# Optimization experiments

Hardware: AMD Instinct MI355X
Metric: run time of the kernel (lower is better)

The kernel has to match this reference:

```python
import jax, jax.numpy as jnp
import numpy as np

B, C, L, E = 32, 3, 512, 512


def setup_inputs() -> dict:
    key = jax.random.key(0)
    ks = jax.random.split(key, 13)
    bnd = float(np.sqrt(6.0 / (2.0 * E)))  # xavier-uniform-like bound
    uni = lambda k, shp: jax.random.uniform(k, shp, jnp.float32, -bnd, bnd)
    return {
        "A0": jax.random.normal(ks[0], (B, C, L, L), jnp.float32),
        "x0": jax.random.normal(ks[1], (B, C, L, E), jnp.float32),
        "u0": jax.random.normal(ks[2], (B, C, E), jnp.float32),
        "t0": jax.random.normal(ks[3], (B, E), jnp.float32),
        "t1": jax.random.normal(ks[4], (B, E), jnp.float32),
        "Q_weight": uni(ks[5], (C, E, E)),
        "Q_bias": jnp.zeros((C, E), jnp.float32),
        "V_weight": uni(ks[6], (C, E, E)),
        "V_bias": jnp.zeros((C, E), jnp.float32),
        "K_weight": uni(ks[7], (C, E, E)),
        "K_bias": jnp.zeros((C, E), jnp.float32),
        "T_weight": uni(ks[8], (C, E, E)),
        "T_bias": jnp.zeros((C, E), jnp.float32),
    }


def reference(A0, x0, u0, t0, t1,
              Q_weight, Q_bias, V_weight, V_bias,
              K_weight, K_bias, T_weight, T_bias):
    # Time embeddings: (B,E) @ (C,E,E) -> (B,C,E)
    T0 = jnp.einsum('be,cef->bcf', t0, T_weight)
    T1 = jnp.einsum('be,cef->bcf', t1, T_weight)

    # Original modulates weight columns: x @ (W * T) == (x @ W) * T (T broadcasts
    # over the input axis via unsqueeze(-2)); use the fused, equivalent form.
    Q = jnp.einsum('bce,cef->bcf', x0[:, :, -1, :], Q_weight) * T0 + Q_bias  # (B,C,E)
    K = jnp.einsum('bce,cef->bcf', u0, K_weight) * T1 + K_bias               # (B,C,E)
    V = jnp.einsum('bcle,cef->bclf', x0, V_weight) * T1[:, :, None, :] \
        + V_bias[None, :, None, :]                                           # (B,C,L,E)

    QKV = jax.nn.softmax(jnp.einsum('bce,bcle->bcl', Q * K, V), axis=-1)     # (B,C,L)

    # A1[:, :, i, :] = A0[:, :, i+1, :] - A0[:, :, 0, :] for i < L-1;
    # A1[:, :, L-1, :] = A1[:, :, L-2, :] + QKV  (= A0[-1] - A0[0] + QKV)
    rows = A0[:, :, 1:, :] - A0[:, :, :1, :]                                 # (B,C,L-1,L)
    last = rows[:, :, -1, :] + QKV                                           # (B,C,L)
    A1 = jnp.concatenate([rows, last[:, :, None, :]], axis=2)                # (B,C,L,L)

    x1 = jnp.einsum('bclm,bcme->bcle', A1, x0)                               # (B,C,L,E)
    x1 = jnp.diff(x1, axis=2, prepend=jnp.zeros_like(x1[:, :, :1, :]))

    num = jnp.sum(T0 * T1, axis=-1)                                          # (B,C)
    den = jnp.sqrt(jnp.sum(T0 * T0, axis=-1) + jnp.sum(T1 * T1, axis=-1))
    w = (num / den)[..., None]                                               # (B,C,1)

    u1 = u0 * (1.0 - w) + x1.mean(axis=-2) * w                               # (B,C,E)
    return (A1 - A0, x1 - x0, u1 - u0)
```

## Files before the change

kernel.cpp:

```cpp
#include <hip/hip_runtime.h>
#include <stdint.h>

#define BB 32
#define CC 3
#define LL 512
#define EE 512
#define NBC (BB*CC)

#define O2_OFF ((size_t)NBC*LL*LL)
#define O3_OFF (O2_OFF + (size_t)NBC*LL*EE)

#define WSB_QX    0
#define WSB_H     196608
#define WSB_W     442368
#define WSB_ADIFF ((size_t)512*1024)
#define ADIFF_BYTES ((size_t)NBC*LL*LL*2)
#define WSB_X0T   (WSB_ADIFF + ADIFF_BYTES)
#define WS_FAST_NEED (WSB_X0T + ADIFF_BYTES)

#define NEC 16

typedef short bf16x8 __attribute__((ext_vector_type(8)));
typedef float f32x4  __attribute__((ext_vector_type(4)));

__device__ __forceinline__ float wred_sum(float v){
#pragma unroll
  for (int m = 32; m >= 1; m >>= 1) v += __shfl_xor(v, m, 64);
  return v;
}
__device__ __forceinline__ float wred_max(float v){
#pragma unroll
  for (int m = 32; m >= 1; m >>= 1) v = fmaxf(v, __shfl_xor(v, m, 64));
  return v;
}
__device__ __forceinline__ void f4ma(float4& a, float s, const float4& b){
  a.x = fmaf(s, b.x, a.x); a.y = fmaf(s, b.y, a.y);
  a.z = fmaf(s, b.z, a.z); a.w = fmaf(s, b.w, a.w);
}
__device__ __forceinline__ float4 f4sub(const float4& a, const float4& b){
  return make_float4(a.x-b.x, a.y-b.y, a.z-b.z, a.w-b.w);
}
__device__ __forceinline__ unsigned short f2bf(float x){
  unsigned u = __float_as_uint(x);
  return (unsigned short)((u + 0x7FFFu + ((u >> 16) & 1u)) >> 16);
}
__device__ __forceinline__ float bf2f(unsigned short h){
  return __uint_as_float(((unsigned)h) << 16);
}
__device__ __forceinline__ void split1(float v, unsigned short& hi, unsigned short& lo){
  hi = f2bf(v);
  lo = f2bf(v - bf2f(hi));
}

__global__ __launch_bounds__(512) void k0p(
    const float* __restrict__ x0, const float* __restrict__ u0,
    const float* __restrict__ t0, const float* __restrict__ t1,
    const float* __restrict__ Qw, const float* __restrict__ Kw,
    const float* __restrict__ Tw,
    float* __restrict__ P)
{
  const int bg = blockIdx.x;
  const int c  = blockIdx.y;
  const int ec = blockIdx.z;
  const int b0 = bg*4;
  const int e0 = ec*32;
  const int f  = threadIdx.x;
  __shared__ float vb[4][4][32];
  {
    int vec = f >> 7, j = (f >> 5) & 3, e = f & 31;
    int bb = b0 + j;
    float v;
    if      (vec == 0) v = t0[bb*EE + e0 + e];
    else if (vec == 1) v = t1[bb*EE + e0 + e];
    else if (vec == 2) v = x0[((size_t)(bb*CC + c)*LL + (LL-1))*EE + e0 + e];
    else               v = u0[(size_t)(bb*CC + c)*EE + e0 + e];
    vb[vec][j][e] = v;
  }
  __syncthreads();

  const float* twp = Tw + (size_t)c*EE*EE + (size_t)e0*EE + f;
  const float* qwp = Qw + (size_t)c*EE*EE + (size_t)e0*EE + f;
  const float* kwp = Kw + (size_t)c*EE*EE + (size_t)e0*EE + f;
  float aT0[4]={0,0,0,0}, aT1[4]={0,0,0,0}, aQ[4]={0,0,0,0}, aK[4]={0,0,0,0};
#pragma unroll 8
  for (int e = 0; e < 32; ++e) {
    float wt = twp[(size_t)e*EE];
    float wq = qwp[(size_t)e*EE];
    float wk = kwp[(size_t)e*EE];
#pragma unroll
    for (int j = 0; j < 4; ++j) {
      aT0[j] = fmaf(vb[0][j][e], wt, aT0[j]);
      aT1[j] = fmaf(vb[1][j][e], wt, aT1[j]);
      aQ[j]  = fmaf(vb[2][j][e], wq, aQ[j]);
      aK[j]  = fmaf(vb[3][j][e], wk, aK[j]);
    }
  }
#pragma unroll
  for (int j = 0; j < 4; ++j) {
    int cb = c*BB + b0 + j;
    P[(((size_t)0*NEC + ec)*96 + cb)*EE + f] = aT0[j];
    P[(((size_t)1*NEC + ec)*96 + cb)*EE + f] = aT1[j];
    P[(((size_t)2*NEC + ec)*96 + cb)*EE + f] = aQ[j];
    P[(((size_t)3*NEC + ec)*96 + cb)*EE + f] = aK[j];
  }
}

__global__ __launch_bounds__(512) void k0c(
    const float* __restrict__ P,
    const float* __restrict__ Qb, const float* __restrict__ Kb,
    float* __restrict__ gtbuf, float* __restrict__ ws_w)
{
  const int bc = blockIdx.x;
  const int b = bc / CC, c = bc % CC;
  const int cb = c*BB + b;
  const int f = threadIdx.x;
  const int wid = f >> 6, lane = f & 63;
  __shared__ float red[8][3];
  float aT0=0.f, aT1=0.f, aQ=0.f, aK=0.f;
#pragma unroll
  for (int ec = 0; ec < NEC; ++ec) {
    aT0 += P[(((size_t)0*NEC + ec)*96 + cb)*EE + f];
    aT1 += P[(((size_t)1*NEC + ec)*96 + cb)*EE + f];
    aQ  += P[(((size_t)2*NEC + ec)*96 + cb)*EE + f];
    aK  += P[(((size_t)3*NEC + ec)*96 + cb)*EE + f];
  }
  float Qv = aQ*aT0 + Qb[c*EE + f];
  float Kv = aK*aT1 + Kb[c*EE + f];
  gtbuf[(size_t)cb*EE + f] = Qv*Kv*aT1;
  float pn = wred_sum(aT0*aT1);
  float p0 = wred_sum(aT0*aT0);
  float p1 = wred_sum(aT1*aT1);
  if (lane == 0) { red[wid][0]=pn; red[wid][1]=p0; red[wid][2]=p1; }
  __syncthreads();
  if (f == 0) {
    float sn=0.f, s0=0.f, s1=0.f;
    for (int i=0;i<8;++i){ sn+=red[i][0]; s0+=red[i][1]; s1+=red[i][2]; }
    ws_w[bc] = sn / sqrtf(s0 + s1);
  }
}

__global__ __launch_bounds__(256) void k1_h(
    const float* __restrict__ Vw, const float* __restrict__ gtbuf,
    float* __restrict__ ws_h)
{
  const int nt = blockIdx.x;
  const int c  = blockIdx.y;
  const int n0 = nt*128;
  const int t = threadIdx.x, lane = t & 63, w = t >> 6;
  __shared__ __align__(16) char AgtH[32*1024];
  __shared__ __align__(16) char AgtL[32*1024];
  __shared__ __align__(16) char BvH[128*128];
  __shared__ __align__(16) char BvL[128*128];
  {
    int row = t >> 3, sl = t & 7;
    const float* src = gtbuf + ((size_t)(c*BB + row))*EE + sl*64;
#pragma unroll
    for (int c3 = 0; c3 < 8; ++c3) {
      float4 a = *reinterpret_cast<const float4*>(src + c3*8);
      float4 b = *reinterpret_cast<const float4*>(src + c3*8 + 4);
      ushort4 h0,h1,l0,l1;
      split1(a.x,h0.x,l0.x); split1(a.y,h0.y,l0.y); split1(a.z,h0.z,l0.z); split1(a.w,h0.w,l0.w);
      split1(b.x,h1.x,l1.x); split1(b.y,h1.y,l1.y); split1(b.z,h1.z,l1.z); split1(b.w,h1.w,l1.w);
      int off = row*1024 + sl*128 + ((c3 ^ (row & 7)) << 4);
      *reinterpret_cast<ushort4*>(AgtH + off)     = h0;
      *reinterpret_cast<ushort4*>(AgtH + off + 8) = h1;
      *reinterpret_cast<ushort4*>(AgtL + off)     = l0;
      *reinterpret_cast<ushort4*>(AgtL + off + 8) = l1;
    }
  }
  f32x4 acc[2][2];
#pragma unroll
  for (int mi=0; mi<2; ++mi)
#pragma unroll
    for (int ni=0; ni<2; ++ni) acc[mi][ni] = (f32x4){0.f,0.f,0.f,0.f};

  for (int kk = 0; kk < 8; ++kk) {
    __syncthreads();
    {
      int nl = t >> 1, half = t & 1;
      const float* src = Vw + (size_t)c*EE*EE + (size_t)(n0+nl)*EE + kk*64 + half*32;
#pragma unroll
      for (int q = 0; q < 4; ++q) {
        float4 a = *reinterpret_cast<const float4*>(src + q*8);
        float4 b = *reinterpret_cast<const float4*>(src + q*8 + 4);
        int c3 = half*4 + q;
        ushort4 h0,h1,l0,l1;
        split1(a.x,h0.x,l0.x); split1(a.y,h0.y,l0.y); split1(a.z,h0.z,l0.z); split1(a.w,h0.w,l0.w);
        split1(b.x,h1.x,l1.x); split1(b.y,h1.y,l1.y); split1(b.z,h1.z,l1.z); split1(b.w,h1.w,l1.w);
        int off = nl*128 + ((c3 ^ (nl & 7)) << 4);
        *reinterpret_cast<ushort4*>(BvH + off)     = h0;
        *reinterpret_cast<ushort4*>(BvH + off + 8) = h1;
        *reinterpret_cast<ushort4*>(BvL + off)     = l0;
        *reinterpret_cast<ushort4*>(BvL + off + 8) = l1;
      }
    }
    __syncthreads();
    bf16x8 afH[2][2], afL[2][2], bfH[2][2], bfL[2][2];
#pragma unroll
    for (int mi=0; mi<2; ++mi)
#pragma unroll
      for (int ks=0; ks<2; ++ks) {
        int row = mi*16 + (lane & 15);
        int c3 = ks*4 + (lane >> 4);
        int off = row*1024 + kk*128 + ((c3 ^ (row & 7)) << 4);
        afH[mi][ks] = *reinterpret_cast<const bf16x8*>(AgtH + off);
        afL[mi][ks] = *reinterpret_cast<const bf16x8*>(AgtL + off);
      }
#pragma unroll
    for (int ni=0; ni<2; ++ni)
#pragma unroll
      for (int ks=0; ks<2; ++ks) {
        int n = w*32 + ni*16 + (lane & 15);
        int c3 = ks*4 + (lane >> 4);
        int off = n*128 + ((c3 ^ (n & 7)) << 4);
        bfH[ni][ks] = *reinterpret_cast<const bf16x8*>(BvH + off);
        bfL[ni][ks] = *reinterpret_cast<const bf16x8*>(BvL + off);
      }
#pragma unroll
    for (int mi=0; mi<2; ++mi)
#pragma unroll
      for (int ni=0; ni<2; ++ni)
#pragma unroll
        for (int ks=0; ks<2; ++ks) {
          acc[mi][ni] = __builtin_amdgcn_mfma_f32_16x16x32_bf16(afH[mi][ks], bfH[ni][ks], acc[mi][ni], 0, 0, 0);
          acc[mi][ni] = __builtin_amdgcn_mfma_f32_16x16x32_bf16(afH[mi][ks], bfL[ni][ks], acc[mi][ni], 0, 0, 0);
          acc[mi][ni] = __builtin_amdgcn_mfma_f32_16x16x32_bf16(afL[mi][ks], bfH[ni][ks], acc[mi][ni], 0, 0, 0);
        }
  }
#pragma unroll
  for (int mi=0; mi<2; ++mi)
#pragma unroll
    for (int ni=0; ni<2; ++ni)
#pragma unroll
      for (int r=0; r<4; ++r) {
        int b = mi*16 + (lane >> 4)*4 + r;
        int e = n0 + w*32 + ni*16 + (lane & 15);
        ws_h[((size_t)(b*CC + c))*EE + e] = acc[mi][ni][r];
      }
}

__global__ __launch_bounds__(512) void k2f(
    const float* __restrict__ A0, const float* __restrict__ x0,
    const float* __restrict__ u0,
    const float* __restrict__ ws_h, const float* __restrict__ ws_w,
    float* __restrict__ ws_qx, float* __restrict__ out1, float* __restrict__ out3)
{
  const int bc = blockIdx.x;
  const int tid = threadIdx.x, wid = tid >> 6, lane = tid & 63;
  __shared__ __align__(16) float hb[EE], sb[LL], a0r0[LL], a0r3[LL];
  __shared__ float red[8];
  __shared__ float partl[4][12][128];
  const size_t abase = (size_t)bc*LL*LL;
  const size_t xbase = (size_t)bc*LL*EE;
  hb[tid]   = ws_h[(size_t)bc*EE + tid];
  a0r0[tid] = A0[abase + tid];
  a0r3[tid] = A0[abase + (size_t)(LL-1)*LL + tid];
  __syncthreads();
  const float4 h0 = *reinterpret_cast<const float4*>(&hb[lane*8]);
  const float4 h1 = *reinterpret_cast<const float4*>(&hb[lane*8+4]);
  for (int l = wid; l < LL; l += 8) {
    const float4* xr = reinterpret_cast<const float4*>(x0 + xbase + (size_t)l*EE);
    float4 v0 = xr[lane*2], v1 = xr[lane*2+1];
    float acc = v0.x*h0.x + v0.y*h0.y + v0.z*h0.z + v0.w*h0.w
              + v1.x*h1.x + v1.y*h1.y + v1.z*h1.z + v1.w*h1.w;
    acc = wred_sum(acc);
    if (lane == 0) sb[l] = acc;
  }
  __syncthreads();
  float v = sb[tid];
  float mx = wred_max(v);
  if (lane == 0) red[wid] = mx;
  __syncthreads();
  mx = red[0];
#pragma unroll
  for (int i = 1; i < 8; ++i) mx = fmaxf(mx, red[i]);
  float ev = __expf(v - mx);
  float sm = wred_sum(ev);
  __syncthreads();
  if (lane == 0) red[wid] = sm;
  __syncthreads();
  float tot = 0.f;
#pragma unroll
  for (int i = 0; i < 8; ++i) tot += red[i];
  float qk = ev / tot;
  sb[tid] = qk;
  out1[abase + (size_t)(LL-1)*LL + tid] = qk - a0r0[tid];
  __syncthreads();
  const int mg = tid >> 7, cg = tid & 127;
  float4 aq = make_float4(0,0,0,0), a0s = make_float4(0,0,0,0), a3s = make_float4(0,0,0,0);
#pragma unroll 4
  for (int i = 0; i < 128; ++i) {
    int m = mg*128 + i;
    float4 xv = *reinterpret_cast<const float4*>(x0 + xbase + (size_t)m*EE + cg*4);
    float qm = sb[m], z0 = a0r0[m], z3 = a0r3[m];
    f4ma(aq, qm, xv); f4ma(a0s, z0, xv); f4ma(a3s, z3, xv);
  }
#pragma unroll
  for (int k = 0; k < 4; ++k) {
    partl[mg][0+k][cg] = (&aq.x)[k];
    partl[mg][4+k][cg] = (&a0s.x)[k];
    partl[mg][8+k][cg] = (&a3s.x)[k];
  }
  __syncthreads();
  if (mg == 0) {
    float wv = ws_w[bc];
    float4 uv = *reinterpret_cast<const float4*>(u0 + (size_t)bc*EE + cg*4);
    float4 qx4, o3;
#pragma unroll
    for (int k = 0; k < 4; ++k) {
      float q = 0.f, y0 = 0.f, y3 = 0.f;
#pragma unroll
      for (int g = 0; g < 4; ++g) {
        q  += partl[g][0+k][cg];
        y0 += partl[g][4+k][cg];
        y3 += partl[g][8+k][cg];
      }
      (&qx4.x)[k] = q;
      (&o3.x)[k] = wv * ((y3 - y0 + q) * (1.f/(float)LL) - (&uv.x)[k]);
    }
    *reinterpret_cast<float4*>(ws_qx + (size_t)bc*EE + cg*4) = qx4;
    *reinterpret_cast<float4*>(out3 + (size_t)bc*EE + cg*4) = o3;
  }
}

__global__ __launch_bounds__(512) void k_conv2(
    const float* __restrict__ A0, const float* __restrict__ x0,
    float* __restrict__ out1, char* __restrict__ adiff, char* __restrict__ x0t)
{
  const int bc = blockIdx.x;
  const int tile = blockIdx.y;
  const int t = threadIdx.x;
  if (blockIdx.z == 0) {
    const int r0 = tile*64;
    const size_t abase = (size_t)bc*LL*LL;
    char* ad = adiff + (size_t)bc*LL*LL*2;
    __shared__ __align__(16) float r0f[LL];
    r0f[t] = A0[abase + t];
    __syncthreads();
#pragma unroll 4
    for (int rep = 0; rep < 16; ++rep) {
      int pos = rep*512 + t;
      int rl = pos >> 7;
      int q  = pos & 127;
      int gr = r0 + rl;
      float4 d;
      if (gr < LL-1) {
        float4 a = *reinterpret_cast<const float4*>(A0 + abase + (size_t)gr*LL + q*4);
        float4 b = *reinterpret_cast<const float4*>(A0 + abase + (size_t)(gr+1)*LL + q*4);
        d = make_float4(b.x-a.x, b.y-a.y, b.z-a.z, b.w-a.w);
        float4 z = *reinterpret_cast<const float4*>(&r0f[q*4]);
        *reinterpret_cast<float4*>(out1 + abase + (size_t)gr*LL + q*4) = f4sub(d, z);
      } else {
        d = make_float4(0.f,0.f,0.f,0.f);
      }
      ushort4 pk;
      pk.x = f2bf(d.x); pk.y = f2bf(d.y); pk.z = f2bf(d.z); pk.w = f2bf(d.w);
      *reinterpret_cast<ushort4*>(ad + (size_t)gr*1024 + q*8) = pk;
    }
  } else {
    const int m0 = tile*64;
    const size_t xbase = (size_t)bc*LL*EE;
    char* xt = x0t + (size_t)bc*LL*EE*2;
    __shared__ float T[64][65];
    for (int ech = 0; ech < 8; ++ech) {
      const int e0 = ech*64;
      {
        int ml = t >> 3, seg = t & 7;
        const float* src = x0 + xbase + (size_t)(m0+ml)*EE + e0 + seg*8;
        float4 v0 = *reinterpret_cast<const float4*>(src);
        float4 v1 = *reinterpret_cast<const float4*>(src+4);
        T[ml][seg*8+0]=v0.x; T[ml][seg*8+1]=v0.y; T[ml][seg*8+2]=v0.z; T[ml][seg*8+3]=v0.w;
        T[ml][seg*8+4]=v1.x; T[ml][seg*8+5]=v1.y; T[ml][seg*8+6]=v1.z; T[ml][seg*8+7]=v1.w;
      }
      __syncthreads();
      {
        int el = t >> 3, c3 = t & 7;
        int eg = e0 + el;
        int mb = c3*8;
        ushort4 p0, p1;
        p0.x = f2bf(T[mb+0][el]); p0.y = f2bf(T[mb+1][el]);
        p0.z = f2bf(T[mb+2][el]); p0.w = f2bf(T[mb+3][el]);
        p1.x = f2bf(T[mb+4][el]); p1.y = f2bf(T[mb+5][el]);
        p1.z = f2bf(T[mb+6][el]); p1.w = f2bf(T[mb+7][el]);
        char* dst = xt + (size_t)eg*1024 + (size_t)(m0 + mb)*2;
        *reinterpret_cast<ushort4*>(dst) = p0;
        *reinterpret_cast<ushort4*>(dst + 8) = p1;
      }
      __syncthreads();
    }
  }
}

#define ASTR 80
__global__ __launch_bounds__(256) void k3_bf(
    const char* __restrict__ adiff, const char* __restrict__ x0t,
    const float* __restrict__ x0, const float* __restrict__ ws_qx,
    float* __restrict__ out2)
{
  const int bc = blockIdx.y;
  const int rt = blockIdx.x >> 2, nt = blockIdx.x & 3;
  const int r0 = rt*128, n0b = nt*128;
  const int t = threadIdx.x;
  const int lane = t & 63, wid = t >> 6;
  const int wr = wid >> 1, wc = wid & 1;
  __shared__ __align__(16) char As[128*ASTR];
  __shared__ __align__(16) char Bs[128*ASTR];
  const char* ad = adiff + (size_t)bc*LL*LL*2;
  const char* xt = x0t  + (size_t)bc*LL*EE*2;
  const size_t xbase = (size_t)bc*LL*EE;
  f32x4 acc[4][4];
#pragma unroll
  for (int mi=0; mi<4; ++mi)
#pragma unroll
    for (int ni=0; ni<4; ++ni) acc[mi][ni] = (f32x4){0.f,0.f,0.f,0.f};

  for (int k0 = 0; k0 < LL; k0 += 32) {
    __syncthreads();
#pragma unroll
    for (int i = 0; i < 2; ++i) {
      int idx = i*256 + t;
      int row = idx >> 2, c = idx & 3;
      int4 v = *reinterpret_cast<const int4*>(ad + (size_t)(r0+row)*1024 + k0*2 + c*16);
      *reinterpret_cast<int4*>(As + row*ASTR + c*16) = v;
    }
#pragma unroll
    for (int i = 0; i < 2; ++i) {
      int idx = i*256 + t;
      int n = idx >> 2, c = idx & 3;
      int4 v = *reinterpret_cast<const int4*>(xt + (size_t)(n0b+n)*1024 + k0*2 + c*16);
      int kb = (c*16) ^ (((n >> 2) & 3) << 4);
      *reinterpret_cast<int4*>(Bs + n*ASTR + kb) = v;
    }
    __syncthreads();
    bf16x8 af[4], bfv[4];
#pragma unroll
    for (int mi=0; mi<4; ++mi) {
      int row = wr*64 + mi*16 + (lane & 15);
      af[mi] = *reinterpret_cast<const bf16x8*>(As + row*ASTR + ((lane>>4)*16));
    }
#pragma unroll
    for (int ni=0; ni<4; ++ni) {
      int n = wc*64 + ni*16 + (lane & 15);
      int kb = ((lane>>4)*16) ^ (((n >> 2) & 3) << 4);
      bfv[ni] = *reinterpret_cast<const bf16x8*>(Bs + n*ASTR + kb);
    }
#pragma unroll
    for (int mi=0; mi<4; ++mi)
#pragma unroll
      for (int ni=0; ni<4; ++ni)
        acc[mi][ni] = __builtin_amdgcn_mfma_f32_16x16x32_bf16(af[mi], bfv[ni], acc[mi][ni], 0, 0, 0);
  }
#pragma unroll
  for (int mi=0; mi<4; ++mi)
#pragma unroll
    for (int r=0; r<4; ++r) {
      int grow = r0 + wr*64 + mi*16 + (lane>>4)*4 + r;
      const size_t rowoff = xbase + (size_t)grow*EE;
#pragma unroll
      for (int ni=0; ni<4; ++ni) {
        int gcol = n0b + wc*64 + ni*16 + (lane & 15);
        float xv = x0[rowoff + gcol];
        float val;
        if (grow == LL-1) val = ws_qx[(size_t)bc*EE + gcol] - xv;
        else              val = acc[mi][ni][r] - xv;
        out2[rowoff + gcol] = val;
      }
    }
}

__global__ __launch_bounds__(512) void kA_fused(
    const float* __restrict__ A0, const float* __restrict__ x0,
    const float* __restrict__ u0,
    const float* __restrict__ t0, const float* __restrict__ t1,
    const float* __restrict__ Qw, const float* __restrict__ Qb,
    const float* __restrict__ Vw,
    const float* __restrict__ Kw, const float* __restrict__ Kb,
    const float* __restrict__ Tw,
    float* __restrict__ ws_qx, float* __restrict__ out1, float* __restrict__ out3)
{
  const int bc = blockIdx.x;
  const int b = bc / CC, c = bc % CC;
  const int tid = threadIdx.x;
  const int wid = tid >> 6, lane = tid & 63;
  __shared__ __align__(16) float t0v[EE], t1v[EE], xl[EE], uv[EE], gt[EE];
  __shared__ __align__(16) float hb[EE], sb[LL], a0r0[LL], a0r3[LL];
  __shared__ float red[3][8];
  __shared__ float wsh;
  const size_t abase = (size_t)bc*LL*LL;
  const size_t xbase = (size_t)bc*LL*EE;

  t0v[tid] = t0[b*EE + tid];
  t1v[tid] = t1[b*EE + tid];
  xl[tid]  = x0[xbase + (size_t)(LL-1)*EE + tid];
  uv[tid]  = u0[(size_t)bc*EE + tid];
  a0r0[tid] = A0[abase + tid];
  a0r3[tid] = A0[abase + (size_t)(LL-1)*LL + tid];
  __syncthreads();

  const int f = tid;
  const float* twp = Tw + (size_t)c*EE*EE + f;
  const float* qwp = Qw + (size_t)c*EE*EE + f;
  const float* kwp = Kw + (size_t)c*EE*EE + f;
  float aT0 = 0.f, aT1 = 0.f, aQ = 0.f, aK = 0.f;
  for (int e = 0; e < EE; ++e) {
    float wt = twp[(size_t)e*EE];
    aT0 = fmaf(t0v[e], wt, aT0);
    aT1 = fmaf(t1v[e], wt, aT1);
    aQ  = fmaf(xl[e],  qwp[(size_t)e*EE], aQ);
    aK  = fmaf(uv[e],  kwp[(size_t)e*EE], aK);
  }
  float Qv = aQ*aT0 + Qb[c*EE + f];
  float Kv = aK*aT1 + Kb[c*EE + f];
  gt[f] = Qv*Kv*aT1;

  float pn = wred_sum(aT0*aT1);
  float p0 = wred_sum(aT0*aT0);
  float p1 = wred_sum(aT1*aT1);
  if (lane == 0) { red[0][wid]=pn; red[1][wid]=p0; red[2][wid]=p1; }
  __syncthreads();
  if (tid == 0) {
    float sn=0.f, s0=0.f, s1=0.f;
    for (int i=0;i<8;++i){ sn+=red[0][i]; s0+=red[1][i]; s1+=red[2][i]; }
    wsh = sn / sqrtf(s0 + s1);
  }
  {
    const float4 g0 = *reinterpret_cast<const float4*>(&gt[lane*8]);
    const float4 g1 = *reinterpret_cast<const float4*>(&gt[lane*8+4]);
    for (int r = wid; r < EE; r += 8) {
      const float4* vr = reinterpret_cast<const float4*>(Vw + ((size_t)c*EE + r)*EE);
      float4 v0 = vr[lane*2], v1 = vr[lane*2+1];
      float acc = v0.x*g0.x + v0.y*g0.y + v0.z*g0.z + v0.w*g0.w
                + v1.x*g1.x + v1.y*g1.y + v1.z*g1.z + v1.w*g1.w;
      acc = wred_sum(acc);
      if (lane == 0) hb[r] = acc;
    }
  }
  __syncthreads();

  {
    const float4 h0 = *reinterpret_cast<const float4*>(&hb[lane*8]);
    const float4 h1 = *reinterpret_cast<const float4*>(&hb[lane*8+4]);
    for (int l = wid; l < LL; l += 8) {
      const float4* xr = reinterpret_cast<const float4*>(x0 + xbase + (size_t)l*EE);
      float4 v0 = xr[lane*2], v1 = xr[lane*2+1];
      float acc = v0.x*h0.x + v0.y*h0.y + v0.z*h0.z + v0.w*h0.w
                + v1.x*h1.x + v1.y*h1.y + v1.z*h1.z + v1.w*h1.w;
      acc = wred_sum(acc);
      if (lane == 0) sb[l] = acc;
    }
  }
  __syncthreads();

  float v = sb[tid];
  float mx = wred_max(v);
  if (lane == 0) red[0][wid] = mx;
  __syncthreads();
  mx = red[0][0];
#pragma unroll
  for (int i = 1; i < 8; ++i) mx = fmaxf(mx, red[0][i]);
  float ev = __expf(v - mx);
  float sm = wred_sum(ev);
  __syncthreads();
  if (lane == 0) red[0][wid] = sm;
  __syncthreads();
  float tot = 0.f;
#pragma unroll
  for (int i = 0; i < 8; ++i) tot += red[0][i];
  float qk = ev / tot;
  sb[tid] = qk;
  out1[abase + (size_t)(LL-1)*LL + tid] = qk - a0r0[tid];
  __syncthreads();

  float qx=0.f, y0=0.f, y3=0.f;
  for (int m = 0; m < LL; ++m) {
    float xm = x0[xbase + (size_t)m*EE + tid];
    qx = fmaf(sb[m],   xm, qx);
    y0 = fmaf(a0r0[m], xm, y0);
    y3 = fmaf(a0r3[m], xm, y3);
  }
  ws_qx[(size_t)bc*EE + tid] = qx;
  float mean = (y3 - y0 + qx) * (1.f/(float)LL);
  out3[(size_t)bc*EE + tid] = wsh * (mean - uv[tid]);
}

__global__ __launch_bounds__(256) void k3_mfma(
    const float* __restrict__ A0, const float* __restrict__ x0,
    const float* __restrict__ ws_qx,
    float* __restrict__ out1, float* __restrict__ out2)
{
  const int bc = blockIdx.y;
  const int rt = blockIdx.x >> 2, nt = blockIdx.x & 3;
  const int r0 = rt*128, n0b = nt*128;
  const int t = threadIdx.x;
  const int lane = t & 63, wid = t >> 6;
  const int wr = wid >> 1, wc = wid & 1;
  __shared__ __align__(16) char As[128*ASTR];
  __shared__ __align__(16) char Bs[128*ASTR];
  const size_t abase = (size_t)bc*LL*LL;
  const size_t xbase = (size_t)bc*LL*EE;
  f32x4 acc[4][4];
#pragma unroll
  for (int mi=0; mi<4; ++mi)
#pragma unroll
    for (int ni=0; ni<4; ++ni) acc[mi][ni] = (f32x4){0.f,0.f,0.f,0.f};
  const int bkl = (t & 7) * 4;
  const int bn0 = (t >> 3) * 4;
  for (int k0 = 0; k0 < LL; k0 += 32) {
    __syncthreads();
#pragma unroll
    for (int i = 0; i < 4; ++i) {
      int idx = i*256 + t;
      int row = idx >> 3, kq = idx & 7;
      int gr = r0 + row;
      int gr1 = (gr+1 > LL-1) ? (LL-1) : (gr+1);
      float4 va = *reinterpret_cast<const float4*>(A0 + abase + (size_t)gr *LL + k0 + kq*4);
      float4 vb = *reinterpret_cast<const float4*>(A0 + abase + (size_t)gr1*LL + k0 + kq*4);
      ushort4 pk;
      pk.x = f2bf(vb.x - va.x); pk.y = f2bf(vb.y - va.y);
      pk.z = f2bf(vb.z - va.z); pk.w = f2bf(vb.w - va.w);
      *reinterpret_cast<ushort4*>(As + row*ASTR + kq*8) = pk;
      if (nt == 0 && gr < LL-1) {
        float4 az = *reinterpret_cast<const float4*>(A0 + abase + k0 + kq*4);
        float4 o = make_float4(vb.x - az.x - va.x, vb.y - az.y - va.y,
                               vb.z - az.z - va.z, vb.w - az.w - va.w);
        *reinterpret_cast<float4*>(out1 + abase + (size_t)gr*LL + k0 + kq*4) = o;
      }
    }
    {
      float xq[4][4];
#pragma unroll
      for (int i = 0; i < 4; ++i)
        *reinterpret_cast<float4*>(xq[i]) =
          *reinterpret_cast<const float4*>(x0 + xbase + (size_t)(k0+bkl+i)*EE + n0b + bn0);
#pragma unroll
      for (int j = 0; j < 4; ++j) {
        int n = bn0 + j;
        ushort4 pk;
        pk.x = f2bf(xq[0][j]); pk.y = f2bf(xq[1][j]);
        pk.z = f2bf(xq[2][j]); pk.w = f2bf(xq[3][j]);
        int kb = (bkl*2) ^ (((n >> 2) & 3) << 4);
        *reinterpret_cast<ushort4*>(Bs + n*ASTR + kb) = pk;
      }
    }
    __syncthreads();
    bf16x8 af[4], bfv[4];
#pragma unroll
    for (int mi=0; mi<4; ++mi) {
      int row = wr*64 + mi*16 + (lane & 15);
      af[mi] = *reinterpret_cast<const bf16x8*>(As + row*ASTR + ((lane>>4)*16));
    }
#pragma unroll
    for (int ni=0; ni<4; ++ni) {
      int n = wc*64 + ni*16 + (lane & 15);
      int kb = ((lane>>4)*16) ^ (((n >> 2) & 3) << 4);
      bfv[ni] = *reinterpret_cast<const bf16x8*>(Bs + n*ASTR + kb);
    }
#pragma unroll
    for (int mi=0; mi<4; ++mi)
#pragma unroll
      for (int ni=0; ni<4; ++ni)
        acc[mi][ni] = __builtin_amdgcn_mfma_f32_16x16x32_bf16(af[mi], bfv[ni], acc[mi][ni], 0, 0, 0);
  }
#pragma unroll
  for (int mi=0; mi<4; ++mi)
#pragma unroll
    for (int r=0; r<4; ++r) {
      int grow = r0 + wr*64 + mi*16 + (lane>>4)*4 + r;
      const size_t rowoff = xbase + (size_t)grow*EE;
#pragma unroll
      for (int ni=0; ni<4; ++ni) {
        int gcol = n0b + wc*64 + ni*16 + (lane & 15);
        float xv = x0[rowoff + gcol];
        float val;
        if (grow == LL-1) val = ws_qx[(size_t)bc*EE + gcol] - xv;
        else              val = acc[mi][ni][r] - xv;
        out2[rowoff + gcol] = val;
      }
    }
}

extern "C" void kernel_launch(void* const* d_in, const int* in_sizes, int n_in,
                              void* d_out, int out_size, void* d_ws, size_t ws_size,
                              hipStream_t stream)
{
  const float* A0 = (const float*)d_in[0];
  const float* x0 = (const float*)d_in[1];
  const float* u0 = (const float*)d_in[2];
  const float* t0 = (const float*)d_in[3];
  const float* t1 = (const float*)d_in[4];
  const float* Qw = (const float*)d_in[5];
  const float* Qb = (const float*)d_in[6];
  const float* Vw = (const float*)d_in[7];
  const float* Kw = (const float*)d_in[9];
  const float* Kb = (const float*)d_in[10];
  const float* Tw = (const float*)d_in[11];

  char*  wsb    = (char*)d_ws;
  float* ws_qx  = (float*)(wsb + WSB_QX);
  float* ws_h   = (float*)(wsb + WSB_H);
  float* ws_w   = (float*)(wsb + WSB_W);

  float* out1 = (float*)d_out;
  float* out2 = out1 + O2_OFF;
  float* out3 = out1 + O3_OFF;
  float* gtbuf = out3;
  float* pscr  = out2;

  const bool fast = ws_size >= WS_FAST_NEED;

  if (fast) {
    char* adiff = wsb + WSB_ADIFF;
    char* x0t   = wsb + WSB_X0T;
    k_conv2<<<dim3(NBC, 8, 2), 512, 0, stream>>>(A0, x0, out1, adiff, x0t);
    k0p<<<dim3(8, 3, NEC), 512, 0, stream>>>(x0, u0, t0, t1, Qw, Kw, Tw, pscr);
    k0c<<<NBC, 512, 0, stream>>>(pscr, Qb, Kb, gtbuf, ws_w);
    k1_h<<<dim3(4, 3), 256, 0, stream>>>(Vw, gtbuf, ws_h);
    k2f<<<NBC, 512, 0, stream>>>(A0, x0, u0, ws_h, ws_w, ws_qx, out1, out3);
    k3_bf<<<dim3(16, NBC), 256, 0, stream>>>(adiff, x0t, x0, ws_qx, out2);
  } else {
    kA_fused<<<NBC, 512, 0, stream>>>(A0, x0, u0, t0, t1, Qw, Qb, Vw, Kw, Kb, Tw,
                                      ws_qx, out1, out3);
    k3_mfma<<<dim3(16, NBC), 256, 0, stream>>>(A0, x0, ws_qx, out1, out2);
  }
}
```

Baseline: 266.5 us.

## Merge conversion and projection-partial kernels into one launch with row reuse

Combines the A0-difference/bf16 conversion, the x0 transpose conversion, and the Q/K/T projection partial-sum kernel into a single 1920-block launch, with blocks dispatched by index range. The A0 path now has each thread walk 16 consecutive rows and carry the previous row in registers, so each A0 row is loaded once instead of twice. The transpose path buffers its packed outputs in registers and writes them all after the loop. Together these remove one launch boundary and redundant A0 reads, at the cost of more registers and shared memory per block, since the union of all three branches' shared arrays is allocated.

```diff
diff --git a/kernel.cpp b/kernel.cpp
--- a/kernel.cpp
+++ b/kernel.cpp
@@ -52,56 +52,139 @@
   lo = f2bf(v - bf2f(hi));
 }
 
-__global__ __launch_bounds__(512) void k0p(
-    const float* __restrict__ x0, const float* __restrict__ u0,
+__global__ __launch_bounds__(512) void conv2m(
+    const float* __restrict__ A0, const float* __restrict__ x0,
+    const float* __restrict__ u0,
     const float* __restrict__ t0, const float* __restrict__ t1,
     const float* __restrict__ Qw, const float* __restrict__ Kw,
     const float* __restrict__ Tw,
+    float* __restrict__ out1, char* __restrict__ adiff, char* __restrict__ x0t,
     float* __restrict__ P)
 {
-  const int bg = blockIdx.x;
-  const int c  = blockIdx.y;
-  const int ec = blockIdx.z;
-  const int b0 = bg*4;
-  const int e0 = ec*32;
-  const int f  = threadIdx.x;
+  const int bid = blockIdx.x;
+  const int t = threadIdx.x;
+  __shared__ __align__(16) float r0f[LL];
+  __shared__ float T[64][65];
   __shared__ float vb[4][4][32];
-  {
-    int vec = f >> 7, j = (f >> 5) & 3, e = f & 31;
-    int bb = b0 + j;
-    float v;
-    if      (vec == 0) v = t0[bb*EE + e0 + e];
-    else if (vec == 1) v = t1[bb*EE + e0 + e];
-    else if (vec == 2) v = x0[((size_t)(bb*CC + c)*LL + (LL-1))*EE + e0 + e];
-    else               v = u0[(size_t)(bb*CC + c)*EE + e0 + e];
-    vb[vec][j][e] = v;
-  }
-  __syncthreads();
-
-  const float* twp = Tw + (size_t)c*EE*EE + (size_t)e0*EE + f;
-  const float* qwp = Qw + (size_t)c*EE*EE + (size_t)e0*EE + f;
-  const float* kwp = Kw + (size_t)c*EE*EE + (size_t)e0*EE + f;
-  float aT0[4]={0,0,0,0}, aT1[4]={0,0,0,0}, aQ[4]={0,0,0,0}, aK[4]={0,0,0,0};
+
+  if (bid < 768) {
+    const int bc = bid >> 3, tile = bid & 7;
+    const int r0 = tile*64;
+    const size_t abase = (size_t)bc*LL*LL;
+    char* ad = adiff + (size_t)bc*LL*LL*2;
+    r0f[t] = A0[abase + t];
+    __syncthreads();
+    const int q = t & 127, rg = t >> 7;
+    const int base = r0 + rg*16;
+    const float4 z = *reinterpret_cast<const float4*>(&r0f[q*4]);
+    float4 prev = *reinterpret_cast<const float4*>(A0 + abase + (size_t)base*LL + q*4);
+#pragma unroll 4
+    for (int i = 0; i < 16; ++i) {
+      int gr = base + i;
+      float4 cur;
+      if (gr + 1 < LL)
+        cur = *reinterpret_cast<const float4*>(A0 + abase + (size_t)(gr+1)*LL + q*4);
+      else
+        cur = prev;
+      float4 d;
+      if (gr < LL-1) {
+        d = f4sub(cur, prev);
+        *reinterpret_cast<float4*>(out1 + abase + (size_t)gr*LL + q*4) = f4sub(d, z);
+      } else {
+        d = make_float4(0.f,0.f,0.f,0.f);
+      }
+      ushort4 pk;
+      pk.x = f2bf(d.x); pk.y = f2bf(d.y); pk.z = f2bf(d.z); pk.w = f2bf(d.w);
+      *reinterpret_cast<ushort4*>(ad + (size_t)gr*1024 + q*8) = pk;
+      prev = cur;
+    }
+  } else if (bid < 1536) {
+    const int bid1 = bid - 768;
+    const int bc = bid1 >> 3, tile = bid1 & 7;
+    const int m0 = tile*64;
+    const size_t xbase = (size_t)bc*LL*EE;
+    char* xt = x0t + (size_t)bc*LL*EE*2;
+    ushort4 outs[8][2];
+#pragma unroll
+    for (int ech = 0; ech < 8; ++ech) {
+      const int e0 = ech*64;
+      {
+        int ml = t >> 3, seg = t & 7;
+        const float* src = x0 + xbase + (size_t)(m0+ml)*EE + e0 + seg*8;
+        float4 v0 = *reinterpret_cast<const float4*>(src);
+        float4 v1 = *reinterpret_cast<const float4*>(src+4);
+        T[ml][seg*8+0]=v0.x; T[ml][seg*8+1]=v0.y; T[ml][seg*8+2]=v0.z; T[ml][seg*8+3]=v0.w;
+        T[ml][seg*8+4]=v1.x; T[ml][seg*8+5]=v1.y; T[ml][seg*8+6]=v1.z; T[ml][seg*8+7]=v1.w;
+      }
+      __syncthreads();
+      {
+        int el = t >> 3, c3 = t & 7;
+        int mb = c3*8;
+        ushort4 p0, p1;
+        p0.x = f2bf(T[mb+0][el]); p0.y = f2bf(T[mb+1][el]);
+        p0.z = f2bf(T[mb+2][el]); p0.w = f2bf(T[mb+3][el]);
+        p1.x = f2bf(T[mb+4][el]); p1.y = f2bf(T[mb+5][el]);
+        p1.z = f2bf(T[mb+6][el]); p1.w = f2bf(T[mb+7][el]);
+        outs[ech][0] = p0;
+        outs[ech][1] = p1;
+      }
+      __syncthreads();
+    }
+    {
+      int el = t >> 3, c3 = t & 7;
+#pragma unroll
+      for (int ech = 0; ech < 8; ++ech) {
+        int eg = ech*64 + el;
+        char* dst = xt + (size_t)eg*1024 + (size_t)(m0 + c3*8)*2;
+        *reinterpret_cast<ushort4*>(dst)     = outs[ech][0];
+        *reinterpret_cast<ushort4*>(dst + 8) = outs[ech][1];
+      }
+    }
+  } else {
+    const int idx = bid - 1536;
+    const int bg = idx & 7;
+    const int rem = idx >> 3;
+    const int c  = rem % 3;
+    const int ec = rem / 3;
+    const int b0 = bg*4;
+    const int e0 = ec*32;
+    const int f  = t;
+    {
+      int vec = f >> 7, j = (f >> 5) & 3, e = f & 31;
+      int bb = b0 + j;
+      float v;
+      if      (vec == 0) v = t0[bb*EE + e0 + e];
+      else if (vec == 1) v = t1[bb*EE + e0 + e];
+      else if (vec == 2) v = x0[((size_t)(bb*CC + c)*LL + (LL-1))*EE + e0 + e];
+      else               v = u0[(size_t)(bb*CC + c)*EE + e0 + e];
+      vb[vec][j][e] = v;
+    }
+    __syncthreads();
+    const float* twp = Tw + (size_t)c*EE*EE + (size_t)e0*EE + f;
+    const float* qwp = Qw + (size_t)c*EE*EE + (size_t)e0*EE + f;
+    const float* kwp = Kw + (size_t)c*EE*EE + (size_t)e0*EE + f;
+    float aT0[4]={0,0,0,0}, aT1[4]={0,0,0,0}, aQ[4]={0,0,0,0}, aK[4]={0,0,0,0};
 #pragma unroll 8
-  for (int e = 0; e < 32; ++e) {
-    float wt = twp[(size_t)e*EE];
-    float wq = qwp[(size_t)e*EE];
-    float wk = kwp[(size_t)e*EE];
+    for (int e = 0; e < 32; ++e) {
+      float wt = twp[(size_t)e*EE];
+      float wq = qwp[(size_t)e*EE];
+      float wk = kwp[(size_t)e*EE];
+#pragma unroll
+      for (int j = 0; j < 4; ++j) {
+        aT0[j] = fmaf(vb[0][j][e], wt, aT0[j]);
+        aT1[j] = fmaf(vb[1][j][e], wt, aT1[j]);
+        aQ[j]  = fmaf(vb[2][j][e], wq, aQ[j]);
+        aK[j]  = fmaf(vb[3][j][e], wk, aK[j]);
+      }
+    }
 #pragma unroll
     for (int j = 0; j < 4; ++j) {
-      aT0[j] = fmaf(vb[0][j][e], wt, aT0[j]);
-      aT1[j] = fmaf(vb[1][j][e], wt, aT1[j]);
-      aQ[j]  = fmaf(vb[2][j][e], wq, aQ[j]);
-      aK[j]  = fmaf(vb[3][j][e], wk, aK[j]);
-    }
-  }
-#pragma unroll
-  for (int j = 0; j < 4; ++j) {
-    int cb = c*BB + b0 + j;
-    P[(((size_t)0*NEC + ec)*96 + cb)*EE + f] = aT0[j];
-    P[(((size_t)1*NEC + ec)*96 + cb)*EE + f] = aT1[j];
-    P[(((size_t)2*NEC + ec)*96 + cb)*EE + f] = aQ[j];
-    P[(((size_t)3*NEC + ec)*96 + cb)*EE + f] = aK[j];
+      int cb = c*BB + b0 + j;
+      P[(((size_t)0*NEC + ec)*96 + cb)*EE + f] = aT0[j];
+      P[(((size_t)1*NEC + ec)*96 + cb)*EE + f] = aT1[j];
+      P[(((size_t)2*NEC + ec)*96 + cb)*EE + f] = aQ[j];
+      P[(((size_t)3*NEC + ec)*96 + cb)*EE + f] = aK[j];
+    }
   }
 }
 
@@ -320,74 +403,6 @@
     }
     *reinterpret_cast<float4*>(ws_qx + (size_t)bc*EE + cg*4) = qx4;
     *reinterpret_cast<float4*>(out3 + (size_t)bc*EE + cg*4) = o3;
-  }
-}
-
-__global__ __launch_bounds__(512) void k_conv2(
-    const float* __restrict__ A0, const float* __restrict__ x0,
-    float* __restrict__ out1, char* __restrict__ adiff, char* __restrict__ x0t)
-{
-  const int bc = blockIdx.x;
-  const int tile = blockIdx.y;
-  const int t = threadIdx.x;
-  if (blockIdx.z == 0) {
-    const int r0 = tile*64;
-    const size_t abase = (size_t)bc*LL*LL;
-    char* ad = adiff + (size_t)bc*LL*LL*2;
-    __shared__ __align__(16) float r0f[LL];
-    r0f[t] = A0[abase + t];
-    __syncthreads();
-#pragma unroll 4
-    for (int rep = 0; rep < 16; ++rep) {
-      int pos = rep*512 + t;
-      int rl = pos >> 7;
-      int q  = pos & 127;
-      int gr = r0 + rl;
-      float4 d;
-      if (gr < LL-1) {
-        float4 a = *reinterpret_cast<const float4*>(A0 + abase + (size_t)gr*LL + q*4);
-        float4 b = *reinterpret_cast<const float4*>(A0 + abase + (size_t)(gr+1)*LL + q*4);
-        d = make_float4(b.x-a.x, b.y-a.y, b.z-a.z, b.w-a.w);
-        float4 z = *reinterpret_cast<const float4*>(&r0f[q*4]);
-        *reinterpret_cast<float4*>(out1 + abase + (size_t)gr*LL + q*4) = f4sub(d, z);
-      } else {
-        d = make_float4(0.f,0.f,0.f,0.f);
-      }
-      ushort4 pk;
-      pk.x = f2bf(d.x); pk.y = f2bf(d.y); pk.z = f2bf(d.z); pk.w = f2bf(d.w);
-      *reinterpret_cast<ushort4*>(ad + (size_t)gr*1024 + q*8) = pk;
-    }
-  } else {
-    const int m0 = tile*64;
-    const size_t xbase = (size_t)bc*LL*EE;
-    char* xt = x0t + (size_t)bc*LL*EE*2;
-    __shared__ float T[64][65];
-    for (int ech = 0; ech < 8; ++ech) {
-      const int e0 = ech*64;
-      {
-        int ml = t >> 3, seg = t & 7;
-        const float* src = x0 + xbase + (size_t)(m0+ml)*EE + e0 + seg*8;
-        float4 v0 = *reinterpret_cast<const float4*>(src);
-        float4 v1 = *reinterpret_cast<const float4*>(src+4);
-        T[ml][seg*8+0]=v0.x; T[ml][seg*8+1]=v0.y; T[ml][seg*8+2]=v0.z; T[ml][seg*8+3]=v0.w;
-        T[ml][seg*8+4]=v1.x; T[ml][seg*8+5]=v1.y; T[ml][seg*8+6]=v1.z; T[ml][seg*8+7]=v1.w;
-      }
-      __syncthreads();
-      {
-        int el = t >> 3, c3 = t & 7;
-        int eg = e0 + el;
-        int mb = c3*8;
-        ushort4 p0, p1;
-        p0.x = f2bf(T[mb+0][el]); p0.y = f2bf(T[mb+1][el]);
-        p0.z = f2bf(T[mb+2][el]); p0.w = f2bf(T[mb+3][el]);
-        p1.x = f2bf(T[mb+4][el]); p1.y = f2bf(T[mb+5][el]);
-        p1.z = f2bf(T[mb+6][el]); p1.w = f2bf(T[mb+7][el]);
-        char* dst = xt + (size_t)eg*1024 + (size_t)(m0 + mb)*2;
-        *reinterpret_cast<ushort4*>(dst) = p0;
-        *reinterpret_cast<ushort4*>(dst + 8) = p1;
-      }
-      __syncthreads();
-    }
   }
 }
 
@@ -711,8 +726,8 @@
   if (fast) {
     char* adiff = wsb + WSB_ADIFF;
     char* x0t   = wsb + WSB_X0T;
-    k_conv2<<<dim3(NBC, 8, 2), 512, 0, stream>>>(A0, x0, out1, adiff, x0t);
-    k0p<<<dim3(8, 3, NEC), 512, 0, stream>>>(x0, u0, t0, t1, Qw, Kw, Tw, pscr);
+    conv2m<<<1920, 512, 0, stream>>>(A0, x0, u0, t0, t1, Qw, Kw, Tw,
+                                     out1, adiff, x0t, pscr);
     k0c<<<NBC, 512, 0, stream>>>(pscr, Qb, Kb, gtbuf, ws_w);
     k1_h<<<dim3(4, 3), 256, 0, stream>>>(Vw, gtbuf, ws_h);
     k2f<<<NBC, 512, 0, stream>>>(A0, x0, u0, ws_h, ws_w, ws_qx, out1, out3);
```

Measured after the change: 268.4 us. About the same (+0.7%).
